# Kernel tuning notes

Measured on AMD Instinct MI355X. Metric: run time of the kernel, lower is better.

Reference implementation:

```python
import jax, jax.numpy as jnp
import numpy as np

N_NODES = 50000
N_EDGES = 800000
N_GRAPHS = 128
D = 128
L = 4
C = 10
GN_EPS = 1e-5


def setup_inputs() -> dict:
    key = jax.random.key(0)
    ks = jax.random.split(key, 12)
    s = 0.05
    x = jax.random.normal(ks[0], (N_NODES, D), dtype=jnp.float32)
    gin_w1 = jax.random.normal(ks[1], (L, D, D), dtype=jnp.float32) * s
    gin_b1 = jax.random.normal(ks[2], (L, D), dtype=jnp.float32) * s
    gin_w2 = jax.random.normal(ks[3], (L, D, D), dtype=jnp.float32) * s
    gin_b2 = jax.random.normal(ks[4], (L, D), dtype=jnp.float32) * s
    gn_weight = jnp.ones((L, D), dtype=jnp.float32)
    gn_bias = jnp.zeros((L, D), dtype=jnp.float32)
    gn_scale = jnp.ones((L, D), dtype=jnp.float32)
    fw1 = jax.random.normal(ks[5], (D, D), dtype=jnp.float32) * s
    fb1 = jnp.zeros((D,), dtype=jnp.float32)
    fw2 = jax.random.normal(ks[6], (D, D), dtype=jnp.float32) * s
    fb2 = jnp.zeros((D,), dtype=jnp.float32)
    fw3 = jax.random.normal(ks[7], (D, C), dtype=jnp.float32) * s
    fb3 = jnp.zeros((C,), dtype=jnp.float32)
    edge_index = jax.random.randint(ks[8], (2, N_EDGES), 0, N_NODES, dtype=jnp.int64)
    batch = jnp.sort(jax.random.randint(ks[9], (N_NODES,), 0, N_GRAPHS, dtype=jnp.int64))
    return dict(x=x, gin_w1=gin_w1, gin_b1=gin_b1, gin_w2=gin_w2, gin_b2=gin_b2,
                gn_weight=gn_weight, gn_bias=gn_bias, gn_scale=gn_scale,
                fw1=fw1, fb1=fb1, fw2=fw2, fb2=fb2, fw3=fw3, fb3=fb3,
                edge_index=edge_index, batch=batch)


def _graph_norm(h, batch, weight, bias, mean_scale, counts):
    # PyG GraphNorm: per-graph mean/var with learnable mean_scale.
    mean = jax.ops.segment_sum(h, batch, num_segments=N_GRAPHS) / counts  # [G, D]
    out = h - mean[batch] * mean_scale
    var = jax.ops.segment_sum(out * out, batch, num_segments=N_GRAPHS) / counts
    return weight * out / jnp.sqrt(var[batch] + GN_EPS) + bias


def reference(x, gin_w1, gin_b1, gin_w2, gin_b2, gn_weight, gn_bias, gn_scale,
              fw1, fb1, fw2, fb2, fw3, fb3, edge_index, batch):
    src, dst = edge_index[0], edge_index[1]
    ones = jnp.ones((N_NODES, 1), dtype=x.dtype)
    counts = jnp.maximum(jax.ops.segment_sum(ones, batch, num_segments=N_GRAPHS), 1.0)  # [G,1]
    h = x
    for l in range(L):
        # GINConv, eps=0: (1+eps)*x + sum_{j->i} x_j, then MLP with act after each Linear
        agg = jax.ops.segment_sum(h[src], dst, num_segments=N_NODES)  # [N, D]
        h = h + agg
        h = jax.nn.relu(h @ gin_w1[l] + gin_b1[l])
        h = jax.nn.relu(h @ gin_w2[l] + gin_b2[l])
        h = _graph_norm(h, batch, gn_weight[l], gn_bias[l], gn_scale[l], counts)
        h = jax.nn.relu(h)
    # sum readout per graph
    g = jax.ops.segment_sum(h, batch, num_segments=N_GRAPHS)  # [G, D]
    # final MLP (dropout is identity in eval)
    g = jax.nn.relu(g @ fw1 + fb1)
    g = jax.nn.relu(g @ fw2 + fb2)
    out = g @ fw3 + fb3
    return jax.nn.log_softmax(out, axis=-1)
```

## Files before the change

### kernel.cpp

```cpp
#include <hip/hip_runtime.h>
#include <cstddef>

#define N_NODES 50000
#define N_EDGES 800000
#define N_GRAPHS 128
#define DIM 128
#define N_LAYERS 4
#define GN_EPS 1e-5f

#define B_CHUNK 256
#define EPB 3125
#define BUCKET_SHIFT 9
#define BUCKET_SIZE 512
#define NB 98

#define CX_BLKS 12500
#define CW_BLKS 512
#define GB_BLKS 196
#define SETUP_BLKS (CX_BLKS + CW_BLKS + GB_BLKS + B_CHUNK)

typedef unsigned short ushort_t;
typedef __attribute__((ext_vector_type(8))) short frag8;
typedef __attribute__((ext_vector_type(4))) float f32x4;

__device__ inline float bfbits2f(unsigned hi16) { return __uint_as_float(hi16 << 16); }
__device__ inline ushort_t bf16rne(float v) {
    unsigned u = __float_as_uint(v);
    unsigned r = u + 0x7fff + ((u >> 16) & 1);
    return (ushort_t)(r >> 16);
}
__device__ inline unsigned packbf2(float a, float b) {
    return (unsigned)bf16rne(a) | ((unsigned)bf16rne(b) << 16);
}
__device__ inline void bf16split(float v, ushort_t& h, ushort_t& l) {
    ushort_t hi = bf16rne(v);
    float fh = __uint_as_float(((unsigned)hi) << 16);
    l = bf16rne(v - fh);
    h = hi;
}

__global__ __launch_bounds__(256) void setup_misc(const float* __restrict__ x, unsigned* __restrict__ Hb,
                                                  const float* __restrict__ w1, const float* __restrict__ w2,
                                                  ushort_t* __restrict__ whi, ushort_t* __restrict__ wlo,
                                                  const int* __restrict__ batch, int* __restrict__ gstart,
                                                  const int* __restrict__ edst, int* __restrict__ cnts) {
    __shared__ int cnt[NB];
    int b = blockIdx.x, t = threadIdx.x;
    if (b < CX_BLKS) {
        int i = b * 256 + t;
        if (i < N_NODES * 64) {
            float a = x[2 * i], bb = x[2 * i + 1];
            Hb[i] = packbf2(a, bb);
        }
    } else if (b < CX_BLKS + CW_BLKS) {
        int idx = (b - CX_BLKS) * 256 + t;
        int mat = idx >> 14;
        int e = idx & 16383;
        int n = e >> 7, k = e & 127;
        int l = mat >> 1;
        const float* src = (mat & 1) ? (w2 + (size_t)l * DIM * DIM) : (w1 + (size_t)l * DIM * DIM);
        float v = src[k * DIM + n];
        ushort_t h, lw;
        bf16split(v, h, lw);
        whi[(size_t)mat * DIM * DIM + n * DIM + k] = h;
        wlo[(size_t)mat * DIM * DIM + n * DIM + k] = lw;
    } else if (b < CX_BLKS + CW_BLKS + GB_BLKS) {
        int i = (b - CX_BLKS - CW_BLKS) * 256 + t;
        if (i < N_NODES) {
            int bb = batch[i];
            if (i == 0) {
                for (int g = 0; g <= bb; ++g) gstart[g] = 0;
            } else {
                int pb = batch[i - 1];
                for (int g = pb + 1; g <= bb; ++g) gstart[g] = i;
            }
            if (i == N_NODES - 1) {
                for (int g = bb + 1; g <= N_GRAPHS; ++g) gstart[g] = N_NODES;
            }
        }
    } else {
        int blk = b - (CX_BLKS + CW_BLKS + GB_BLKS);
        for (int i = t; i < NB; i += 256) cnt[i] = 0;
        __syncthreads();
        int base = blk * EPB;
        for (int i = t; i < EPB; i += 256) atomicAdd(&cnt[edst[base + i] >> BUCKET_SHIFT], 1);
        __syncthreads();
        for (int i = t; i < NB; i += 256) cnts[i * B_CHUNK + blk] = cnt[i];
    }
}

__global__ __launch_bounds__(1024) void scan_local(const int* __restrict__ in, int* __restrict__ out,
                                                   int* __restrict__ bsum, int n) {
    __shared__ int wsum[16];
    int tid = threadIdx.x, lane = tid & 63, w = tid >> 6;
    int gi = blockIdx.x * 1024 + tid;
    int v = (gi < n) ? in[gi] : 0;
    int s = v;
    #pragma unroll
    for (int off = 1; off < 64; off <<= 1) {
        int t = __shfl_up(s, off, 64);
        if (lane >= off) s += t;
    }
    if (lane == 63) wsum[w] = s;
    __syncthreads();
    if (w == 0) {
        int ws = (lane < 16) ? wsum[lane] : 0;
        #pragma unroll
        for (int off = 1; off < 16; off <<= 1) {
            int t = __shfl_up(ws, off, 64);
            if (lane >= off) ws += t;
        }
        if (lane < 16) wsum[lane] = ws;
    }
    __syncthreads();
    int woff = (w > 0) ? wsum[w - 1] : 0;
    if (gi < n) out[gi] = woff + s - v;
    if (tid == 1023) bsum[blockIdx.x] = woff + s;
}

__global__ __launch_bounds__(1024) void scan_add(int* __restrict__ out, const int* __restrict__ bsum,
                                                 int n, int total) {
    int lane = threadIdx.x & 63;
    int v = (lane < (int)blockIdx.x) ? bsum[lane] : 0;
    #pragma unroll
    for (int off = 1; off < 64; off <<= 1) v += __shfl_xor(v, off, 64);
    int gi = blockIdx.x * 1024 + threadIdx.x;
    if (gi < n) out[gi] += v;
    if (blockIdx.x == 0 && threadIdx.x == 0) out[n] = total;
}

__global__ __launch_bounds__(256) void p3_place(const int* __restrict__ src, const int* __restrict__ dst,
                                                const int* __restrict__ off, unsigned* __restrict__ ebuf) {
    __shared__ int cur[NB];
    int t = threadIdx.x, blk = blockIdx.x;
    for (int i = t; i < NB; i += 256) cur[i] = off[i * B_CHUNK + blk];
    __syncthreads();
    int base = blk * EPB;
    for (int i = t; i < EPB; i += 256) {
        int d = dst[base + i];
        int b = d >> BUCKET_SHIFT;
        int pos = atomicAdd(&cur[b], 1);
        ebuf[pos] = (unsigned)src[base + i] | ((unsigned)(d & (BUCKET_SIZE - 1)) << 16);
    }
}

__global__ __launch_bounds__(512) void p4_csr(const unsigned* __restrict__ ebuf, const int* __restrict__ off,
                                              int* __restrict__ eoff, int* __restrict__ csr) {
    __shared__ int cnt[BUCKET_SIZE];
    __shared__ int wsum[8];
    int k = blockIdx.x, t = threadIdx.x;
    int bstart = off[k * B_CHUNK];
    int bend = off[(k + 1) * B_CHUNK];
    cnt[t] = 0;
    __syncthreads();
    for (int i = bstart + t; i < bend; i += 512) atomicAdd(&cnt[ebuf[i] >> 16], 1);
    __syncthreads();
    int lane = t & 63, w = t >> 6;
    int v = cnt[t], s = v;
    #pragma unroll
    for (int o = 1; o < 64; o <<= 1) {
        int tt = __shfl_up(s, o, 64);
        if (lane >= o) s += tt;
    }
    if (lane == 63) wsum[w] = s;
    __syncthreads();
    if (w == 0) {
        int ws = (lane < 8) ? wsum[lane] : 0;
        #pragma unroll
        for (int o = 1; o < 8; o <<= 1) {
            int tt = __shfl_up(ws, o, 64);
            if (lane >= o) ws += tt;
        }
        if (lane < 8) wsum[lane] = ws;
    }
    __syncthreads();
    int woff = (w > 0) ? wsum[w - 1] : 0;
    int excl = woff + s - v;
    int node = k * BUCKET_SIZE + t;
    if (node < N_NODES) eoff[node] = bstart + excl;
    __syncthreads();
    cnt[t] = excl;
    __syncthreads();
    for (int i = bstart + t; i < bend; i += 512) {
        unsigned p = ebuf[i];
        int pos = atomicAdd(&cnt[p >> 16], 1);
        csr[bstart + pos] = (int)(p & 0xffffu);
    }
    if (k == NB - 1 && t == 0) eoff[N_NODES] = N_EDGES;
}

__global__ __launch_bounds__(256) void agg_bf16(const uint4* __restrict__ h4, const int* __restrict__ eoff,
                                                const int* __restrict__ csr, uint4* __restrict__ T4) {
    int wid = (blockIdx.x * 256 + threadIdx.x) >> 6;
    int lane = threadIdx.x & 63;
    int qtr = lane >> 4;
    int ql = lane & 15;
    if (wid >= N_NODES) return;
    int lo = eoff[wid], hi = eoff[wid + 1];

    float a[8];
    #pragma unroll
    for (int k = 0; k < 8; ++k) a[k] = 0.f;

    auto acc_row = [&](uint4 w) {
        a[0] += bfbits2f(w.x & 0xffffu); a[1] += bfbits2f(w.x >> 16);
        a[2] += bfbits2f(w.y & 0xffffu); a[3] += bfbits2f(w.y >> 16);
        a[4] += bfbits2f(w.z & 0xffffu); a[5] += bfbits2f(w.z >> 16);
        a[6] += bfbits2f(w.w & 0xffffu); a[7] += bfbits2f(w.w >> 16);
    };

    if (qtr == 0) acc_row(h4[(size_t)wid * 16 + ql]);

    for (int base = lo; base < hi; base += 64) {
        int nav = hi - base;
        if (nav > 64) nav = 64;
        int jv = (base + lane < hi) ? csr[base + lane] : 0;
        int cmin = nav >> 2;
        int cmax = (nav + 3) >> 2;
        int i = 0;
        for (; i + 3 < cmin; i += 4) {
            int j0 = __shfl(jv, 4 * (i + 0) + qtr, 64);
            int j1 = __shfl(jv, 4 * (i + 1) + qtr, 64);
            int j2 = __shfl(jv, 4 * (i + 2) + qtr, 64);
            int j3 = __shfl(jv, 4 * (i + 3) + qtr, 64);
            uint4 w0 = h4[(size_t)j0 * 16 + ql];
            uint4 w1 = h4[(size_t)j1 * 16 + ql];
            uint4 w2 = h4[(size_t)j2 * 16 + ql];
            uint4 w3 = h4[(size_t)j3 * 16 + ql];
            acc_row(w0); acc_row(w1); acc_row(w2); acc_row(w3);
        }
        for (; i < cmin; ++i) {
            int j = __shfl(jv, 4 * i + qtr, 64);
            acc_row(h4[(size_t)j * 16 + ql]);
        }
        for (; i < cmax; ++i) {
            int epos = 4 * i + qtr;
            int j = __shfl(jv, epos, 64);
            if (epos < nav) acc_row(h4[(size_t)j * 16 + ql]);
        }
    }

    #pragma unroll
    for (int k = 0; k < 8; ++k) {
        a[k] += __shfl_down(a[k], 32, 64);
        a[k] += __shfl_down(a[k], 16, 64);
    }
    if (qtr == 0) {
        uint4 o;
        o.x = packbf2(a[0], a[1]);
        o.y = packbf2(a[2], a[3]);
        o.z = packbf2(a[4], a[5]);
        o.w = packbf2(a[6], a[7]);
        T4[(size_t)wid * 16 + ql] = o;
    }
}

__global__ __launch_bounds__(512) void mm_layer(const ushort_t* __restrict__ A,
                                                const ushort_t* __restrict__ W1h, const ushort_t* __restrict__ W1l,
                                                const ushort_t* __restrict__ W2h, const ushort_t* __restrict__ W2l,
                                                const float* __restrict__ b1, const float* __restrict__ b2,
                                                ushort_t* __restrict__ Zb) {
    __shared__ ushort_t As[256 * 128];
    __shared__ ushort_t Ws[128 * 128];
    int tid = threadIdx.x;
    int row0 = blockIdx.x * 256;
    int wave = tid >> 6, lane = tid & 63;
    int q = lane >> 4, mn = lane & 15;

    f32x4 acc[2][8];
    #pragma unroll
    for (int t = 0; t < 2; ++t)
        #pragma unroll
        for (int n = 0; n < 8; ++n) acc[t][n] = (f32x4)(0.f);

    #pragma unroll
    for (int i = 0; i < 8; ++i) {
        int c = tid + i * 512;
        int r = c >> 4, c8 = c & 15;
        uint4 v = make_uint4(0u, 0u, 0u, 0u);
        int gr = row0 + r;
        if (gr < N_NODES) v = *(const uint4*)(A + (size_t)gr * DIM + c8 * 8);
        *(uint4*)(&As[r * 128 + (c8 ^ (r & 7)) * 8]) = v;
    }
    auto stageW = [&](const ushort_t* src) {
        #pragma unroll
        for (int i = 0; i < 4; ++i) {
            int c = tid + i * 512;
            int r = c >> 4, c8 = c & 15;
            uint4 v = *(const uint4*)(src + r * DIM + c8 * 8);
            *(uint4*)(&Ws[r * 128 + (c8 ^ (r & 7)) * 8]) = v;
        }
    };
    auto compute = [&]() {
        #pragma unroll
        for (int ks = 0; ks < 4; ++ks) {
            int m0 = wave * 32 + mn;
            int m1 = m0 + 16;
            frag8 a0 = *(const frag8*)&As[m0 * 128 + (((ks * 4 + q) ^ (m0 & 7)) * 8)];
            frag8 a1 = *(const frag8*)&As[m1 * 128 + (((ks * 4 + q) ^ (m1 & 7)) * 8)];
            #pragma unroll
            for (int n = 0; n < 8; ++n) {
                int nr = n * 16 + mn;
                frag8 b = *(const frag8*)&Ws[nr * 128 + (((ks * 4 + q) ^ (nr & 7)) * 8)];
                acc[0][n] = __builtin_amdgcn_mfma_f32_16x16x32_bf16(a0, b, acc[0][n], 0, 0, 0);
                acc[1][n] = __builtin_amdgcn_mfma_f32_16x16x32_bf16(a1, b, acc[1][n], 0, 0, 0);
            }
        }
    };

    stageW(W1h);
    __syncthreads(); compute(); __syncthreads();
    stageW(W1l);
    __syncthreads(); compute(); __syncthreads();

    int mloc = wave * 32;
    #pragma unroll
    for (int t = 0; t < 2; ++t) {
        #pragma unroll
        for (int n = 0; n < 8; ++n) {
            int col = n * 16 + mn;
            float bv = b1[col];
            #pragma unroll
            for (int r = 0; r < 4; ++r) {
                int rloc = mloc + t * 16 + q * 4 + r;
                float v = fmaxf(acc[t][n][r] + bv, 0.f);
                As[rloc * 128 + ((col >> 3) ^ (rloc & 7)) * 8 + (col & 7)] = bf16rne(v);
                acc[t][n][r] = 0.f;
            }
        }
    }
    __syncthreads();
    stageW(W2h);
    __syncthreads(); compute(); __syncthreads();
    stageW(W2l);
    __syncthreads(); compute();

    #pragma unroll
    for (int t = 0; t < 2; ++t) {
        #pragma unroll
        for (int n = 0; n < 8; ++n) {
            int col = n * 16 + mn;
            float bv = b2[col];
            #pragma unroll
            for (int r = 0; r < 4; ++r) {
                int grow = row0 + mloc + t * 16 + q * 4 + r;
                if (grow < N_NODES)
                    Zb[(size_t)grow * DIM + col] = bf16rne(fmaxf(acc[t][n][r] + bv, 0.f));
            }
        }
    }
}

__global__ __launch_bounds__(1024) void gn_fused(const unsigned* __restrict__ Zb, const int* __restrict__ gstart,
                                                 const float* __restrict__ scale, const float* __restrict__ weight,
                                                 const float* __restrict__ bias,
                                                 unsigned* __restrict__ Hb) {
    __shared__ f32x4 sh1[1024], sh2[1024];
    __shared__ float sa[64], sb[64];
    int g = blockIdx.x >> 1, half = blockIdx.x & 1;
    int t = threadIdx.x;
    int uld = t & 15, rg = t >> 4;
    int s = gstart[g], e = gstart[g + 1];
    const unsigned* zp = Zb + half * 32 + uld * 2;
    f32x4 s1 = (f32x4)(0.f), s2 = (f32x4)(0.f);
    for (int n = s + rg; n < e; n += 64) {
        uint2 zz = *(const uint2*)(zp + (size_t)n * 64);
        f32x4 z;
        z[0] = bfbits2f(zz.x & 0xffffu); z[1] = bfbits2f(zz.x >> 16);
        z[2] = bfbits2f(zz.y & 0xffffu); z[3] = bfbits2f(zz.y >> 16);
        s1 += z;
        s2 += z * z;
    }
    sh1[t] = s1;
    sh2[t] = s2;
    __syncthreads();
    int dbase = half * 64 + uld * 4;
    if (rg == 0) {
        #pragma unroll 8
        for (int k = 1; k < 64; ++k) { s1 += sh1[uld + 16 * k]; s2 += sh2[uld + 16 * k]; }
        int cnt = e - s;
        float cf = (float)(cnt > 0 ? cnt : 1);
        #pragma unroll
        for (int j = 0; j < 4; ++j) {
            float m = s1[j] / cf, ez = s2[j] / cf;
            float sc = scale[dbase + j];
            float var = fmaxf(ez - (2.0f - sc) * sc * m * m, 0.f);
            sa[uld * 4 + j] = m * sc;
            sb[uld * 4 + j] = weight[dbase + j] / sqrtf(var + GN_EPS);
        }
    }
    __syncthreads();
    float as0 = sa[uld * 4], as1 = sa[uld * 4 + 1], as2 = sa[uld * 4 + 2], as3 = sa[uld * 4 + 3];
    float bm0 = sb[uld * 4], bm1 = sb[uld * 4 + 1], bm2 = sb[uld * 4 + 2], bm3 = sb[uld * 4 + 3];
    float bi0 = bias[dbase], bi1 = bias[dbase + 1], bi2 = bias[dbase + 2], bi3 = bias[dbase + 3];
    unsigned* hp = Hb + half * 32 + uld * 2;
    for (int n = s + rg; n < e; n += 64) {
        uint2 zz = *(const uint2*)(zp + (size_t)n * 64);
        float z0 = bfbits2f(zz.x & 0xffffu), z1 = bfbits2f(zz.x >> 16);
        float z2 = bfbits2f(zz.y & 0xffffu), z3 = bfbits2f(zz.y >> 16);
        float o0 = fmaxf((z0 - as0) * bm0 + bi0, 0.f);
        float o1 = fmaxf((z1 - as1) * bm1 + bi1, 0.f);
        float o2 = fmaxf((z2 - as2) * bm2 + bi2, 0.f);
        float o3 = fmaxf((z3 - as3) * bm3 + bi3, 0.f);
        uint2 o;
        o.x = packbf2(o0, o1);
        o.y = packbf2(o2, o3);
        *(uint2*)(hp + (size_t)n * 64) = o;
    }
}

__global__ __launch_bounds__(1024) void gn_last(const unsigned* __restrict__ Zb, const int* __restrict__ gstart,
                                                const float* __restrict__ scale, const float* __restrict__ weight,
                                                const float* __restrict__ bias,
                                                const float* __restrict__ fw1, const float* __restrict__ fb1,
                                                const float* __restrict__ fw2, const float* __restrict__ fb2,
                                                const float* __restrict__ fw3, const float* __restrict__ fb3,
                                                float* __restrict__ out) {
    __shared__ f32x4 sh1[1024], sh2[1024];
    __shared__ float sa[128], sb[128];
    __shared__ float v0[128], v1[128], v2[128], lg[10];
    int g = blockIdx.x;
    int t = threadIdx.x;
    int du = t & 31, rg = t >> 5;
    int s = gstart[g], e = gstart[g + 1];
    const unsigned* zp = Zb + du * 2;
    f32x4 s1 = (f32x4)(0.f), s2 = (f32x4)(0.f);
    for (int n = s + rg; n < e; n += 32) {
        uint2 zz = *(const uint2*)(zp + (size_t)n * 64);
        f32x4 z;
        z[0] = bfbits2f(zz.x & 0xffffu); z[1] = bfbits2f(zz.x >> 16);
        z[2] = bfbits2f(zz.y & 0xffffu); z[3] = bfbits2f(zz.y >> 16);
        s1 += z;
        s2 += z * z;
    }
    sh1[t] = s1;
    sh2[t] = s2;
    __syncthreads();
    int dbase = du * 4;
    if (rg == 0) {
        #pragma unroll 8
        for (int k = 1; k < 32; ++k) { s1 += sh1[du + 32 * k]; s2 += sh2[du + 32 * k]; }
        int cnt = e - s;
        float cf = (float)(cnt > 0 ? cnt : 1);
        #pragma unroll
        for (int j = 0; j < 4; ++j) {
            float m = s1[j] / cf, ez = s2[j] / cf;
            float sc = scale[dbase + j];
            float var = fmaxf(ez - (2.0f - sc) * sc * m * m, 0.f);
            sa[dbase + j] = m * sc;
            sb[dbase + j] = weight[dbase + j] / sqrtf(var + GN_EPS);
        }
    }
    __syncthreads();
    float as_[4], bm_[4], bi_[4];
    #pragma unroll
    for (int j = 0; j < 4; ++j) {
        as_[j] = sa[dbase + j];
        bm_[j] = sb[dbase + j];
        bi_[j] = bias[dbase + j];
    }
    f32x4 rsum = (f32x4)(0.f);
    for (int n = s + rg; n < e; n += 32) {
        uint2 zz = *(const uint2*)(zp + (size_t)n * 64);
        float z0 = bfbits2f(zz.x & 0xffffu), z1 = bfbits2f(zz.x >> 16);
        float z2 = bfbits2f(zz.y & 0xffffu), z3 = bfbits2f(zz.y >> 16);
        rsum[0] += fmaxf((z0 - as_[0]) * bm_[0] + bi_[0], 0.f);
        rsum[1] += fmaxf((z1 - as_[1]) * bm_[1] + bi_[1], 0.f);
        rsum[2] += fmaxf((z2 - as_[2]) * bm_[2] + bi_[2], 0.f);
        rsum[3] += fmaxf((z3 - as_[3]) * bm_[3] + bi_[3], 0.f);
    }
    __syncthreads();
    sh1[t] = rsum;
    __syncthreads();
    if (rg == 0) {
        #pragma unroll 8
        for (int k = 1; k < 32; ++k) rsum += sh1[du + 32 * k];
        #pragma unroll
        for (int j = 0; j < 4; ++j) v0[dbase + j] = rsum[j];
    }
    __syncthreads();
    if (t < 128) {
        float acc = fb1[t];
        for (int d = 0; d < 128; ++d) acc += v0[d] * fw1[d * 128 + t];
        v1[t] = fmaxf(acc, 0.f);
    }
    __syncthreads();
    if (t < 128) {
        float acc = fb2[t];
        for (int d = 0; d < 128; ++d) acc += v1[d] * fw2[d * 128 + t];
        v2[t] = fmaxf(acc, 0.f);
    }
    __syncthreads();
    if (t < 10) {
        float acc = fb3[t];
        for (int d = 0; d < 128; ++d) acc += v2[d] * fw3[d * 10 + t];
        lg[t] = acc;
    }
    __syncthreads();
    if (t < 10) {
        float m = -1e30f;
        for (int c = 0; c < 10; ++c) m = fmaxf(m, lg[c]);
        float ssum = 0.f;
        for (int c = 0; c < 10; ++c) ssum += expf(lg[c] - m);
        out[g * 10 + t] = lg[t] - m - logf(ssum);
    }
}

extern "C" void kernel_launch(void* const* d_in, const int* in_sizes, int n_in,
                              void* d_out, int out_size, void* d_ws, size_t ws_size,
                              hipStream_t stream) {
    const float* x      = (const float*)d_in[0];
    const float* gin_w1 = (const float*)d_in[1];
    const float* gin_b1 = (const float*)d_in[2];
    const float* gin_w2 = (const float*)d_in[3];
    const float* gin_b2 = (const float*)d_in[4];
    const float* gn_w   = (const float*)d_in[5];
    const float* gn_b   = (const float*)d_in[6];
    const float* gn_s   = (const float*)d_in[7];
    const float* fw1    = (const float*)d_in[8];
    const float* fb1    = (const float*)d_in[9];
    const float* fw2    = (const float*)d_in[10];
    const float* fb2    = (const float*)d_in[11];
    const float* fw3    = (const float*)d_in[12];
    const float* fb3    = (const float*)d_in[13];
    const int*   eidx   = (const int*)d_in[14];
    const int*   batch  = (const int*)d_in[15];
    float* out = (float*)d_out;

    const int* esrc = eidx;
    const int* edst = eidx + N_EDGES;

    auto align_up = [](size_t v) { return (v + 255) & ~(size_t)255; };
    char* p = (char*)d_ws;
    unsigned* Hb = (unsigned*)p;   p += align_up((size_t)N_NODES * DIM * 2);
    unsigned* Tb = (unsigned*)p;   p += align_up((size_t)N_NODES * DIM * 2);
    unsigned* Zb = (unsigned*)p;   p += align_up((size_t)N_NODES * DIM * 2);
    ushort_t* WThi = (ushort_t*)p; p += align_up((size_t)8 * DIM * DIM * 2);
    ushort_t* WTlo = (ushort_t*)p; p += align_up((size_t)8 * DIM * DIM * 2);
    int* gstart = (int*)p;         p += align_up((N_GRAPHS + 1) * 4);
    int* cnts = (int*)p;           p += align_up((size_t)NB * B_CHUNK * 4);
    int* off = (int*)p;            p += align_up(((size_t)NB * B_CHUNK + 1) * 4);
    int* bsum = (int*)p;           p += align_up(64 * 4);
    unsigned* ebuf = (unsigned*)p; p += align_up((size_t)N_EDGES * 4);
    int* eoff = (int*)p;           p += align_up((N_NODES + 1) * 4);
    int* csr = (int*)p;            p += align_up((size_t)N_EDGES * 4);

    const int SCAN_N = NB * B_CHUNK;
    const int SCAN_BLKS = (SCAN_N + 1023) / 1024;
    setup_misc<<<SETUP_BLKS, 256, 0, stream>>>(x, Hb, gin_w1, gin_w2, WThi, WTlo,
                                               batch, gstart, edst, cnts);
    scan_local<<<SCAN_BLKS, 1024, 0, stream>>>(cnts, off, bsum, SCAN_N);
    scan_add<<<SCAN_BLKS, 1024, 0, stream>>>(off, bsum, SCAN_N, N_EDGES);
    p3_place<<<B_CHUNK, 256, 0, stream>>>(esrc, edst, off, ebuf);
    p4_csr<<<NB, 512, 0, stream>>>(ebuf, off, eoff, csr);

    const int mm_grid = (N_NODES + 255) / 256;
    for (int l = 0; l < N_LAYERS; ++l) {
        agg_bf16<<<(N_NODES + 3) / 4, 256, 0, stream>>>((const uint4*)Hb, eoff, csr, (uint4*)Tb);
        mm_layer<<<mm_grid, 512, 0, stream>>>((const ushort_t*)Tb,
            WThi + (size_t)(2 * l) * DIM * DIM, WTlo + (size_t)(2 * l) * DIM * DIM,
            WThi + (size_t)(2 * l + 1) * DIM * DIM, WTlo + (size_t)(2 * l + 1) * DIM * DIM,
            gin_b1 + l * DIM, gin_b2 + l * DIM, (ushort_t*)Zb);
        if (l == N_LAYERS - 1)
            gn_last<<<N_GRAPHS, 1024, 0, stream>>>(Zb, gstart, gn_s + l * DIM,
                gn_w + l * DIM, gn_b + l * DIM, fw1, fb1, fw2, fb2, fw3, fb3, out);
        else
            gn_fused<<<N_GRAPHS * 2, 1024, 0, stream>>>(Zb, gstart, gn_s + l * DIM,
                gn_w + l * DIM, gn_b + l * DIM, Hb);
    }
}
```

Baseline: 382.4 us.

## Fuse GraphNorm statistics into matmul epilogue and drop scan_add kernel

The per-graph sum and sum-of-squares for GraphNorm are now accumulated in the mm_layer epilogue, using shared-memory atomics for up to eight local graphs and global atomics otherwise. The statistics buffer is zeroed inside agg_bf16. This replaces the two-pass gn_fused kernel with a flat, fully parallel gn_norm pass, and gn_last no longer reduces statistics itself. The scan_add kernel is removed by having p3_place and p4_csr add the block prefix themselves. The cost is atomic traffic, extra shared memory in the matmul kernel that may lower occupancy, and run-to-run nondeterminism in float summation order.

```diff
diff --git a/kernel.cpp b/kernel.cpp
--- a/kernel.cpp
+++ b/kernel.cpp
@@ -13,11 +13,14 @@
 #define BUCKET_SHIFT 9
 #define BUCKET_SIZE 512
 #define NB 98
+#define SCAN_BLKS 25
 
 #define CX_BLKS 12500
 #define CW_BLKS 512
 #define GB_BLKS 196
 #define SETUP_BLKS (CX_BLKS + CW_BLKS + GB_BLKS + B_CHUNK)
+
+#define LG 8
 
 typedef unsigned short ushort_t;
 typedef __attribute__((ext_vector_type(8))) short frag8;
@@ -118,22 +121,27 @@
     if (tid == 1023) bsum[blockIdx.x] = woff + s;
 }
 
-__global__ __launch_bounds__(1024) void scan_add(int* __restrict__ out, const int* __restrict__ bsum,
-                                                 int n, int total) {
-    int lane = threadIdx.x & 63;
-    int v = (lane < (int)blockIdx.x) ? bsum[lane] : 0;
-    #pragma unroll
-    for (int off = 1; off < 64; off <<= 1) v += __shfl_xor(v, off, 64);
-    int gi = blockIdx.x * 1024 + threadIdx.x;
-    if (gi < n) out[gi] += v;
-    if (blockIdx.x == 0 && threadIdx.x == 0) out[n] = total;
-}
-
 __global__ __launch_bounds__(256) void p3_place(const int* __restrict__ src, const int* __restrict__ dst,
-                                                const int* __restrict__ off, unsigned* __restrict__ ebuf) {
+                                                const int* __restrict__ off, const int* __restrict__ bsum,
+                                                unsigned* __restrict__ ebuf) {
     __shared__ int cur[NB];
+    __shared__ int pexc[32];
     int t = threadIdx.x, blk = blockIdx.x;
-    for (int i = t; i < NB; i += 256) cur[i] = off[i * B_CHUNK + blk];
+    if (t < 32) {
+        int v = (t < SCAN_BLKS) ? bsum[t] : 0;
+        int sI = v;
+        #pragma unroll
+        for (int o = 1; o < 32; o <<= 1) {
+            int u = __shfl_up(sI, o, 64);
+            if (t >= o) sI += u;
+        }
+        pexc[t] = sI - v;
+    }
+    __syncthreads();
+    for (int i = t; i < NB; i += 256) {
+        int j = i * B_CHUNK + blk;
+        cur[i] = off[j] + pexc[j >> 10];
+    }
     __syncthreads();
     int base = blk * EPB;
     for (int i = t; i < EPB; i += 256) {
@@ -145,14 +153,27 @@
 }
 
 __global__ __launch_bounds__(512) void p4_csr(const unsigned* __restrict__ ebuf, const int* __restrict__ off,
+                                              const int* __restrict__ bsum,
                                               int* __restrict__ eoff, int* __restrict__ csr) {
     __shared__ int cnt[BUCKET_SIZE];
     __shared__ int wsum[8];
+    __shared__ int pexc[32];
     int k = blockIdx.x, t = threadIdx.x;
-    int bstart = off[k * B_CHUNK];
-    int bend = off[(k + 1) * B_CHUNK];
+    if (t < 32) {
+        int v = (t < SCAN_BLKS) ? bsum[t] : 0;
+        int sI = v;
+        #pragma unroll
+        for (int o = 1; o < 32; o <<= 1) {
+            int u = __shfl_up(sI, o, 64);
+            if (t >= o) sI += u;
+        }
+        pexc[t] = sI - v;
+    }
     cnt[t] = 0;
     __syncthreads();
+    int bstart = off[k * B_CHUNK] + pexc[(k * B_CHUNK) >> 10];
+    int bend = (k == NB - 1) ? N_EDGES
+                             : off[(k + 1) * B_CHUNK] + pexc[((k + 1) * B_CHUNK) >> 10];
     for (int i = bstart + t; i < bend; i += 512) atomicAdd(&cnt[ebuf[i] >> 16], 1);
     __syncthreads();
     int lane = t & 63, w = t >> 6;
@@ -190,7 +211,10 @@
 }
 
 __global__ __launch_bounds__(256) void agg_bf16(const uint4* __restrict__ h4, const int* __restrict__ eoff,
-                                                const int* __restrict__ csr, uint4* __restrict__ T4) {
+                                                const int* __restrict__ csr, uint4* __restrict__ T4,
+                                                float* __restrict__ Sstat) {
+    int zi = blockIdx.x * 256 + threadIdx.x;
+    if (zi < 2 * N_GRAPHS * DIM) Sstat[zi] = 0.f;
     int wid = (blockIdx.x * 256 + threadIdx.x) >> 6;
     int lane = threadIdx.x & 63;
     int qtr = lane >> 4;
@@ -259,9 +283,13 @@
                                                 const ushort_t* __restrict__ W1h, const ushort_t* __restrict__ W1l,
                                                 const ushort_t* __restrict__ W2h, const ushort_t* __restrict__ W2l,
                                                 const float* __restrict__ b1, const float* __restrict__ b2,
+                                                const int* __restrict__ batch,
+                                                float* __restrict__ S1, float* __restrict__ S2,
                                                 ushort_t* __restrict__ Zb) {
     __shared__ ushort_t As[256 * 128];
     __shared__ ushort_t Ws[128 * 128];
+    __shared__ float lst[LG][DIM][2];
+    __shared__ int gmap[256];
     int tid = threadIdx.x;
     int row0 = blockIdx.x * 256;
     int wave = tid >> 6, lane = tid & 63;
@@ -282,6 +310,12 @@
         if (gr < N_NODES) v = *(const uint4*)(A + (size_t)gr * DIM + c8 * 8);
         *(uint4*)(&As[r * 128 + (c8 ^ (r & 7)) * 8]) = v;
     }
+    if (tid < 256) {
+        int gr = row0 + tid;
+        gmap[tid] = batch[gr < N_NODES ? gr : (N_NODES - 1)];
+    }
+    for (int i = tid; i < LG * DIM * 2; i += 512) ((float*)lst)[i] = 0.f;
+
     auto stageW = [&](const ushort_t* src) {
         #pragma unroll
         for (int i = 0; i < 4; ++i) {
@@ -335,120 +369,138 @@
     stageW(W2l);
     __syncthreads(); compute();
 
+    int gbase = gmap[0];
     #pragma unroll
     for (int t = 0; t < 2; ++t) {
         #pragma unroll
         for (int n = 0; n < 8; ++n) {
             int col = n * 16 + mn;
             float bv = b2[col];
+            float vv[4];
             #pragma unroll
             for (int r = 0; r < 4; ++r) {
-                int grow = row0 + mloc + t * 16 + q * 4 + r;
+                int rloc = mloc + t * 16 + q * 4 + r;
+                int grow = row0 + rloc;
+                float v = fmaxf(acc[t][n][r] + bv, 0.f);
+                vv[r] = v;
                 if (grow < N_NODES)
-                    Zb[(size_t)grow * DIM + col] = bf16rne(fmaxf(acc[t][n][r] + bv, 0.f));
+                    Zb[(size_t)grow * DIM + col] = bf16rne(v);
             }
-        }
-    }
-}
-
-__global__ __launch_bounds__(1024) void gn_fused(const unsigned* __restrict__ Zb, const int* __restrict__ gstart,
-                                                 const float* __restrict__ scale, const float* __restrict__ weight,
-                                                 const float* __restrict__ bias,
-                                                 unsigned* __restrict__ Hb) {
-    __shared__ f32x4 sh1[1024], sh2[1024];
-    __shared__ float sa[64], sb[64];
-    int g = blockIdx.x >> 1, half = blockIdx.x & 1;
-    int t = threadIdx.x;
-    int uld = t & 15, rg = t >> 4;
-    int s = gstart[g], e = gstart[g + 1];
-    const unsigned* zp = Zb + half * 32 + uld * 2;
-    f32x4 s1 = (f32x4)(0.f), s2 = (f32x4)(0.f);
-    for (int n = s + rg; n < e; n += 64) {
-        uint2 zz = *(const uint2*)(zp + (size_t)n * 64);
-        f32x4 z;
-        z[0] = bfbits2f(zz.x & 0xffffu); z[1] = bfbits2f(zz.x >> 16);
-        z[2] = bfbits2f(zz.y & 0xffffu); z[3] = bfbits2f(zz.y >> 16);
-        s1 += z;
-        s2 += z * z;
-    }
-    sh1[t] = s1;
-    sh2[t] = s2;
-    __syncthreads();
-    int dbase = half * 64 + uld * 4;
-    if (rg == 0) {
-        #pragma unroll 8
-        for (int k = 1; k < 64; ++k) { s1 += sh1[uld + 16 * k]; s2 += sh2[uld + 16 * k]; }
-        int cnt = e - s;
-        float cf = (float)(cnt > 0 ? cnt : 1);
-        #pragma unroll
-        for (int j = 0; j < 4; ++j) {
-            float m = s1[j] / cf, ez = s2[j] / cf;
-            float sc = scale[dbase + j];
+            int rb = mloc + t * 16;
+            bool span16 = (row0 + rb + 15 < N_NODES) && (gmap[rb] == gmap[rb + 15]);
+            if (span16) {
+                float s = vv[0] + vv[1] + vv[2] + vv[3];
+                float s2 = vv[0]*vv[0] + vv[1]*vv[1] + vv[2]*vv[2] + vv[3]*vv[3];
+                s += __shfl_xor(s, 16, 64);  s += __shfl_xor(s, 32, 64);
+                s2 += __shfl_xor(s2, 16, 64); s2 += __shfl_xor(s2, 32, 64);
+                if (q == 0) {
+                    int lg = gmap[rb] - gbase;
+                    if (lg < LG) {
+                        atomicAdd(&lst[lg][col][0], s);
+                        atomicAdd(&lst[lg][col][1], s2);
+                    } else {
+                        atomicAdd(&S1[gmap[rb] * DIM + col], s);
+                        atomicAdd(&S2[gmap[rb] * DIM + col], s2);
+                    }
+                }
+            } else {
+                #pragma unroll
+                for (int r = 0; r < 4; ++r) {
+                    int rl = rb + q * 4 + r;
+                    int grow = row0 + rl;
+                    if (grow < N_NODES) {
+                        int g = gmap[rl];
+                        int lg = g - gbase;
+                        float v = vv[r];
+                        if (lg >= 0 && lg < LG) {
+                            atomicAdd(&lst[lg][col][0], v);
+                            atomicAdd(&lst[lg][col][1], v * v);
+                        } else {
+                            atomicAdd(&S1[g * DIM + col], v);
+                            atomicAdd(&S2[g * DIM + col], v * v);
+                        }
+                    }
+                }
+            }
+        }
+    }
+    __syncthreads();
+    for (int i = tid; i < LG * DIM; i += 512) {
+        int lg = i >> 7, d = i & 127;
+        float a1 = lst[lg][d][0], a2 = lst[lg][d][1];
+        if (a1 != 0.f || a2 != 0.f) {
+            int g = gbase + lg;
+            atomicAdd(&S1[g * DIM + d], a1);
+            atomicAdd(&S2[g * DIM + d], a2);
+        }
+    }
+}
+
+__global__ __launch_bounds__(256) void gn_norm(const uint4* __restrict__ Zb4,
+                                               const float* __restrict__ S1, const float* __restrict__ S2,
+                                               const int* __restrict__ batch, const int* __restrict__ gstart,
+                                               const float* __restrict__ scale, const float* __restrict__ weight,
+                                               const float* __restrict__ bias,
+                                               uint4* __restrict__ Hb4) {
+    int idx = blockIdx.x * 256 + threadIdx.x;
+    int n = idx >> 4, c = idx & 15, d0 = c * 8;
+    int g = batch[n];
+    int cnt = gstart[g + 1] - gstart[g];
+    float cf = (float)(cnt > 0 ? cnt : 1);
+    uint4 zz = Zb4[idx];
+    unsigned zw[4] = {zz.x, zz.y, zz.z, zz.w};
+    const float* s1p = S1 + (size_t)g * DIM + d0;
+    const float* s2p = S2 + (size_t)g * DIM + d0;
+    unsigned ow[4];
+    #pragma unroll
+    for (int p = 0; p < 4; ++p) {
+        float o2[2];
+        #pragma unroll
+        for (int h = 0; h < 2; ++h) {
+            int j = p * 2 + h;
+            float m = s1p[j] / cf, ez = s2p[j] / cf;
+            float sc = scale[d0 + j];
             float var = fmaxf(ez - (2.0f - sc) * sc * m * m, 0.f);
-            sa[uld * 4 + j] = m * sc;
-            sb[uld * 4 + j] = weight[dbase + j] / sqrtf(var + GN_EPS);
-        }
-    }
-    __syncthreads();
-    float as0 = sa[uld * 4], as1 = sa[uld * 4 + 1], as2 = sa[uld * 4 + 2], as3 = sa[uld * 4 + 3];
-    float bm0 = sb[uld * 4], bm1 = sb[uld * 4 + 1], bm2 = sb[uld * 4 + 2], bm3 = sb[uld * 4 + 3];
-    float bi0 = bias[dbase], bi1 = bias[dbase + 1], bi2 = bias[dbase + 2], bi3 = bias[dbase + 3];
-    unsigned* hp = Hb + half * 32 + uld * 2;
-    for (int n = s + rg; n < e; n += 64) {
-        uint2 zz = *(const uint2*)(zp + (size_t)n * 64);
-        float z0 = bfbits2f(zz.x & 0xffffu), z1 = bfbits2f(zz.x >> 16);
-        float z2 = bfbits2f(zz.y & 0xffffu), z3 = bfbits2f(zz.y >> 16);
-        float o0 = fmaxf((z0 - as0) * bm0 + bi0, 0.f);
-        float o1 = fmaxf((z1 - as1) * bm1 + bi1, 0.f);
-        float o2 = fmaxf((z2 - as2) * bm2 + bi2, 0.f);
-        float o3 = fmaxf((z3 - as3) * bm3 + bi3, 0.f);
-        uint2 o;
-        o.x = packbf2(o0, o1);
-        o.y = packbf2(o2, o3);
-        *(uint2*)(hp + (size_t)n * 64) = o;
-    }
+            float av = m * sc;
+            float bm = weight[d0 + j] / sqrtf(var + GN_EPS);
+            float z = bfbits2f(h ? (zw[p] >> 16) : (zw[p] & 0xffffu));
+            o2[h] = fmaxf((z - av) * bm + bias[d0 + j], 0.f);
+        }
+        ow[p] = packbf2(o2[0], o2[1]);
+    }
+    uint4 o;
+    o.x = ow[0]; o.y = ow[1]; o.z = ow[2]; o.w = ow[3];
+    Hb4[idx] = o;
 }
 
 __global__ __launch_bounds__(1024) void gn_last(const unsigned* __restrict__ Zb, const int* __restrict__ gstart,
+                                                const float* __restrict__ S1, const float* __restrict__ S2,
                                                 const float* __restrict__ scale, const float* __restrict__ weight,
                                                 const float* __restrict__ bias,
                                                 const float* __restrict__ fw1, const float* __restrict__ fb1,
                                                 const float* __restrict__ fw2, const float* __restrict__ fb2,
                                                 const float* __restrict__ fw3, const float* __restrict__ fb3,
                                                 float* __restrict__ out) {
-    __shared__ f32x4 sh1[1024], sh2[1024];
+    __shared__ f32x4 sh1[1024];
     __shared__ float sa[128], sb[128];
     __shared__ float v0[128], v1[128], v2[128], lg[10];
     int g = blockIdx.x;
     int t = threadIdx.x;
     int du = t & 31, rg = t >> 5;
     int s = gstart[g], e = gstart[g + 1];
-    const unsigned* zp = Zb + du * 2;
-    f32x4 s1 = (f32x4)(0.f), s2 = (f32x4)(0.f);
-    for (int n = s + rg; n < e; n += 32) {
-        uint2 zz = *(const uint2*)(zp + (size_t)n * 64);
-        f32x4 z;
-        z[0] = bfbits2f(zz.x & 0xffffu); z[1] = bfbits2f(zz.x >> 16);
-        z[2] = bfbits2f(zz.y & 0xffffu); z[3] = bfbits2f(zz.y >> 16);
-        s1 += z;
-        s2 += z * z;
-    }
-    sh1[t] = s1;
-    sh2[t] = s2;
-    __syncthreads();
     int dbase = du * 4;
     if (rg == 0) {
-        #pragma unroll 8
-        for (int k = 1; k < 32; ++k) { s1 += sh1[du + 32 * k]; s2 += sh2[du + 32 * k]; }
         int cnt = e - s;
         float cf = (float)(cnt > 0 ? cnt : 1);
         #pragma unroll
         for (int j = 0; j < 4; ++j) {
-            float m = s1[j] / cf, ez = s2[j] / cf;
-            float sc = scale[dbase + j];
+            int d = dbase + j;
+            float m = S1[(size_t)g * DIM + d] / cf;
+            float ez = S2[(size_t)g * DIM + d] / cf;
+            float sc = scale[d];
             float var = fmaxf(ez - (2.0f - sc) * sc * m * m, 0.f);
-            sa[dbase + j] = m * sc;
-            sb[dbase + j] = weight[dbase + j] / sqrtf(var + GN_EPS);
+            sa[d] = m * sc;
+            sb[d] = weight[d] / sqrtf(var + GN_EPS);
         }
     }
     __syncthreads();
@@ -459,6 +511,7 @@
         bm_[j] = sb[dbase + j];
         bi_[j] = bias[dbase + j];
     }
+    const unsigned* zp = Zb + du * 2;
     f32x4 rsum = (f32x4)(0.f);
     for (int n = s + rg; n < e; n += 32) {
         uint2 zz = *(const uint2*)(zp + (size_t)n * 64);
@@ -469,7 +522,6 @@
         rsum[2] += fmaxf((z2 - as_[2]) * bm_[2] + bi_[2], 0.f);
         rsum[3] += fmaxf((z3 - as_[3]) * bm_[3] + bi_[3], 0.f);
     }
-    __syncthreads();
     sh1[t] = rsum;
     __syncthreads();
     if (rg == 0) {
@@ -537,6 +589,7 @@
     unsigned* Zb = (unsigned*)p;   p += align_up((size_t)N_NODES * DIM * 2);
     ushort_t* WThi = (ushort_t*)p; p += align_up((size_t)8 * DIM * DIM * 2);
     ushort_t* WTlo = (ushort_t*)p; p += align_up((size_t)8 * DIM * DIM * 2);
+    float* Sstat = (float*)p;      p += align_up((size_t)2 * N_GRAPHS * DIM * 4);
     int* gstart = (int*)p;         p += align_up((N_GRAPHS + 1) * 4);
     int* cnts = (int*)p;           p += align_up((size_t)NB * B_CHUNK * 4);
     int* off = (int*)p;            p += align_up(((size_t)NB * B_CHUNK + 1) * 4);
@@ -545,27 +598,28 @@
     int* eoff = (int*)p;           p += align_up((N_NODES + 1) * 4);
     int* csr = (int*)p;            p += align_up((size_t)N_EDGES * 4);
 
+    float* S1 = Sstat;
+    float* S2 = Sstat + N_GRAPHS * DIM;
+
     const int SCAN_N = NB * B_CHUNK;
-    const int SCAN_BLKS = (SCAN_N + 1023) / 1024;
     setup_misc<<<SETUP_BLKS, 256, 0, stream>>>(x, Hb, gin_w1, gin_w2, WThi, WTlo,
                                                batch, gstart, edst, cnts);
     scan_local<<<SCAN_BLKS, 1024, 0, stream>>>(cnts, off, bsum, SCAN_N);
-    scan_add<<<SCAN_BLKS, 1024, 0, stream>>>(off, bsum, SCAN_N, N_EDGES);
-    p3_place<<<B_CHUNK, 256, 0, stream>>>(esrc, edst, off, ebuf);
-    p4_csr<<<NB, 512, 0, stream>>>(ebuf, off, eoff, csr);
+    p3_place<<<B_CHUNK, 256, 0, stream>>>(esrc, edst, off, bsum, ebuf);
+    p4_csr<<<NB, 512, 0, stream>>>(ebuf, off, bsum, eoff, csr);
 
     const int mm_grid = (N_NODES + 255) / 256;
     for (int l = 0; l < N_LAYERS; ++l) {
-        agg_bf16<<<(N_NODES + 3) / 4, 256, 0, stream>>>((const uint4*)Hb, eoff, csr, (uint4*)Tb);
+        agg_bf16<<<(N_NODES + 3) / 4, 256, 0, stream>>>((const uint4*)Hb, eoff, csr, (uint4*)Tb, Sstat);
         mm_layer<<<mm_grid, 512, 0, stream>>>((const ushort_t*)Tb,
             WThi + (size_t)(2 * l) * DIM * DIM, WTlo + (size_t)(2 * l) * DIM * DIM,
             WThi + (size_t)(2 * l + 1) * DIM * DIM, WTlo + (size_t)(2 * l + 1) * DIM * DIM,
-            gin_b1 + l * DIM, gin_b2 + l * DIM, (ushort_t*)Zb);
+            gin_b1 + l * DIM, gin_b2 + l * DIM, batch, S1, S2, (ushort_t*)Zb);
         if (l == N_LAYERS - 1)
-            gn_last<<<N_GRAPHS, 1024, 0, stream>>>(Zb, gstart, gn_s + l * DIM,
+            gn_last<<<N_GRAPHS, 1024, 0, stream>>>(Zb, gstart, S1, S2, gn_s + l * DIM,
                 gn_w + l * DIM, gn_b + l * DIM, fw1, fb1, fw2, fb2, fw3, fb3, out);
         else
-            gn_fused<<<N_GRAPHS * 2, 1024, 0, stream>>>(Zb, gstart, gn_s + l * DIM,
-                gn_w + l * DIM, gn_b + l * DIM, Hb);
-    }
-}
+            gn_norm<<<(N_NODES * 16) / 256, 256, 0, stream>>>((const uint4*)Zb, S1, S2,
+                batch, gstart, gn_s + l * DIM, gn_w + l * DIM, gn_b + l * DIM, (uint4*)Hb);
+    }
+}
```

Result: slower. 437.2 us (+14.3%).
